# Kernel tuning notes

Measured on AMD Instinct MI355X. Metric: run time of the kernel, lower is better.

Reference implementation:

```python
import jax, jax.numpy as jnp
import numpy as np
import math

R = 3; NTOT = 100000; N0 = 80000; N1 = 20000; B = 4096
E1 = 300000; E2 = 65536
F_IN = 128; HID = 128; H1 = 2; OUT = 128
HC1 = H1 * HID   # 256
HC2 = OUT        # 128 (heads=1 in layer 2)


def setup_inputs() -> dict:
    key = jax.random.key(0)
    ks = jax.random.split(key, 40)
    w = lambda i, shape: (jax.random.normal(ks[i], shape, jnp.float32) * 0.05)
    inp = {}
    inp['features'] = jax.random.normal(ks[0], (NTOT, F_IN), jnp.float32)
    inp['n_ids'] = jax.random.randint(ks[1], (R, N0), 0, NTOT)
    src1 = jax.random.randint(ks[2], (R, 1, E1), 0, N0)
    dst1 = jax.random.randint(ks[3], (R, 1, E1), 0, N1)
    inp['ei1'] = jnp.concatenate([src1, dst1], axis=1)
    src2 = jax.random.randint(ks[4], (R, 1, E2), 0, N1)
    dst2 = jax.random.randint(ks[5], (R, 1, E2), 0, B)
    inp['ei2'] = jnp.concatenate([src2, dst2], axis=1)
    inp['wq1'] = w(6, (R, F_IN, HC1)); inp['bq1'] = w(7, (R, HC1))
    inp['wk1'] = w(8, (R, F_IN, HC1)); inp['bk1'] = w(9, (R, HC1))
    inp['wv1'] = w(10, (R, F_IN, HC1)); inp['bv1'] = w(11, (R, HC1))
    inp['ws1'] = w(12, (R, F_IN, HC1)); inp['bs1'] = w(13, (R, HC1))
    inp['wbeta1'] = w(14, (R, 3 * HC1, 1))
    # batchnorm (eval mode, running stats)
    inp['bn_g'] = jax.random.uniform(ks[15], (R, HC1), jnp.float32, 0.5, 1.5)
    inp['bn_b'] = w(16, (R, HC1))
    inp['bn_m'] = w(17, (R, HC1))
    inp['bn_v'] = jax.random.uniform(ks[18], (R, HC1), jnp.float32, 0.5, 1.5)
    inp['wq2'] = w(19, (R, HC1, HC2)); inp['bq2'] = w(20, (R, HC2))
    inp['wk2'] = w(21, (R, HC1, HC2)); inp['bk2'] = w(22, (R, HC2))
    inp['wv2'] = w(23, (R, HC1, HC2)); inp['bv2'] = w(24, (R, HC2))
    inp['ws2'] = w(25, (R, HC1, HC2)); inp['bs2'] = w(26, (R, HC2))
    inp['wbeta2'] = w(27, (R, 3 * HC2, 1))
    return inp


def transformer_conv(x_src, x_dst, src, dst, wq, bq, wk, bk, wv, bv, ws, bs, wbeta, H, C, Nt):
    """PyG TransformerConv, bipartite, concat=True, beta=True, eval (no dropout)."""
    q = (x_dst @ wq + bq).reshape(-1, H, C)   # [Nt, H, C]
    k = (x_src @ wk + bk).reshape(-1, H, C)   # [Ns, H, C]
    v = (x_src @ wv + bv).reshape(-1, H, C)
    # per-edge attention logits
    alpha = jnp.einsum('ehc,ehc->eh', q[dst], k[src]) / math.sqrt(C)  # [E, H]
    amax = jax.ops.segment_max(alpha, dst, num_segments=Nt)           # [Nt, H]
    amax = jnp.where(jnp.isfinite(amax), amax, 0.0)
    p = jnp.exp(alpha - amax[dst])
    denom = jax.ops.segment_sum(p, dst, num_segments=Nt)              # [Nt, H]
    p = p / denom[dst]
    out = jax.ops.segment_sum(p[:, :, None] * v[src], dst, num_segments=Nt)
    out = out.reshape(Nt, H * C)
    x_r = x_dst @ ws + bs                                             # skip connection
    beta = jax.nn.sigmoid(jnp.concatenate([out, x_r, out - x_r], -1) @ wbeta)  # [Nt,1]
    return beta * x_r + (1.0 - beta) * out


def reference(features, n_ids, ei1, ei2,
              wq1, bq1, wk1, bk1, wv1, bv1, ws1, bs1, wbeta1,
              bn_g, bn_b, bn_m, bn_v,
              wq2, bq2, wk2, bk2, wv2, bv2, ws2, bs2, wbeta2):
    outs = []
    for r in range(R):
        x = features[n_ids[r]]                 # [N0, 128]
        h = transformer_conv(x, x[:N1], ei1[r, 0], ei1[r, 1],
                             wq1[r], bq1[r], wk1[r], bk1[r], wv1[r], bv1[r],
                             ws1[r], bs1[r], wbeta1[r], H1, HID, N1)  # [N1, 256]
        h = (h - bn_m[r]) * jax.lax.rsqrt(bn_v[r] + 1e-5) * bn_g[r] + bn_b[r]
        h = jax.nn.elu(h)
        o = transformer_conv(h, h[:B], ei2[r, 0], ei2[r, 1],
                             wq2[r], bq2[r], wk2[r], bk2[r], wv2[r], bv2[r],
                             ws2[r], bs2[r], wbeta2[r], 1, OUT, B)    # [B, 128]
        outs.append(o)
    feats = jnp.stack(outs, 0)                 # [R, B, 128]
    return jnp.transpose(feats, (1, 0, 2)).reshape(B, R * OUT)
```

## Files before the change

kernel.cpp:

```cpp
#include <hip/hip_runtime.h>
#include <math.h>

#define RR 3
#define NTOT 100000
#define NN0 80000
#define NN1 20000
#define NB 4096
#define NE1 300000
#define NE2 65536
#define FIN 128
#define HC1 256
#define HC2 128

typedef __attribute__((ext_vector_type(8))) short bf16x8;
typedef __attribute__((ext_vector_type(4))) short s16x4;
typedef __attribute__((ext_vector_type(2))) short s16x2;
typedef __attribute__((ext_vector_type(4))) float f32x4;
typedef __attribute__((ext_vector_type(2))) float f32x2;

__device__ __forceinline__ float wave_red_sum(float v) {
    #pragma unroll
    for (int off = 32; off >= 1; off >>= 1) v += __shfl_xor(v, off, 64);
    return v;
}

__device__ __forceinline__ short f2bf(float x) {
    union { float f; unsigned u; } c; c.f = x;
    unsigned r = c.u + 0x7fffu + ((c.u >> 16) & 1u);
    return (short)(r >> 16);
}
__device__ __forceinline__ float bf2f(short s) {
    union { unsigned u; float f; } c; c.u = ((unsigned)(unsigned short)s) << 16;
    return c.f;
}

__device__ __forceinline__ float4 dec_fp8x4(unsigned w) {
    f32x2 lo = __builtin_amdgcn_cvt_pk_f32_fp8((int)w, false);
    f32x2 hi = __builtin_amdgcn_cvt_pk_f32_fp8((int)w, true);
    float4 r = { lo[0], lo[1], hi[0], hi[1] };
    return r;
}
__device__ __forceinline__ float2 dec_fp8x2(unsigned w) {
    f32x2 lo = __builtin_amdgcn_cvt_pk_f32_fp8((int)w, false);
    float2 r = { lo[0], lo[1] };
    return r;
}
__device__ __forceinline__ unsigned enc_fp8x4(float a, float b, float c, float d) {
    int w = __builtin_amdgcn_cvt_pk_fp8_f32(a, b, 0, false);
    w = __builtin_amdgcn_cvt_pk_fp8_f32(c, d, w, true);
    return (unsigned)w;
}

__device__ __forceinline__ float4 ld4(const float* p) { return *(const float4*)p; }
__device__ __forceinline__ float4 ld4(const short* p) {
    s16x4 v = *(const s16x4*)p;
    float4 r = { bf2f(v[0]), bf2f(v[1]), bf2f(v[2]), bf2f(v[3]) };
    return r;
}
__device__ __forceinline__ float2 ld2(const float* p) { return *(const float2*)p; }
__device__ __forceinline__ float2 ld2(const short* p) {
    s16x2 v = *(const s16x2*)p;
    float2 r = { bf2f(v[0]), bf2f(v[1]) };
    return r;
}

__global__ void __launch_bounds__(256)
fcvt_k(const float* __restrict__ f, short* __restrict__ o, int n4) {
    int i = blockIdx.x * 256 + threadIdx.x;
    if (i < n4) {
        float4 v = *(const float4*)(f + (size_t)i * 4);
        s16x4 s = { f2bf(v.x), f2bf(v.y), f2bf(v.z), f2bf(v.w) };
        *(s16x4*)(o + (size_t)i * 4) = s;
    }
}

template<int K, int N>
__global__ void __launch_bounds__(256)
wpack_k(const float* __restrict__ W0, const float* __restrict__ W1,
        const float* __restrict__ W2, const float* __restrict__ W3,
        short* __restrict__ P) {
    constexpr int KS = K / 32;
    const int m = blockIdx.y, r = blockIdx.z;
    const float* W = (m == 0 ? W0 : m == 1 ? W1 : m == 2 ? W2 : W3) + (size_t)r * K * N;
    short* o = P + ((size_t)(r * 4 + m)) * K * N;
    for (int i = blockIdx.x * 256 + threadIdx.x; i < K * N; i += gridDim.x * 256) {
        int j = i & 7, lane = (i >> 3) & 63, f = i >> 9;
        int ks = f % KS, nt = f / KS;
        int k = ks * 32 + (lane >> 4) * 8 + j;
        int n = nt * 16 + (lane & 15);
        o[i] = f2bf(W[(size_t)k * N + n]);
    }
}

template<int K, int N, typename OT0, typename OT1>
__global__ void __launch_bounds__(256)
gemm2l(const short* __restrict__ xbf, int ldx, const int* __restrict__ gidx,
       const short* __restrict__ P0, const float* __restrict__ b0, OT0* __restrict__ out0,
       const short* __restrict__ P1, const float* __restrict__ b1, OT1* __restrict__ out1)
{
    constexpr int NT = N / 16;
    constexpr int NW = NT / 4;
    constexpr int KS = K / 32;
    constexpr int MT = 2;
    const int lane = threadIdx.x & 63;
    const int wid  = threadIdx.x >> 6;
    const int rowbase = blockIdx.x * (MT * 16);

    const short* ap[MT];
    #pragma unroll
    for (int mt = 0; mt < MT; ++mt) {
        int arow = rowbase + mt * 16 + (lane & 15);
        int srow = gidx ? gidx[arow] : arow;
        ap[mt] = xbf + (size_t)srow * ldx + ((lane >> 4) * 8);
    }
    const int fb = lane * 8;

    f32x4 acc[MT][NW][2];
    #pragma unroll
    for (int mt = 0; mt < MT; ++mt)
        #pragma unroll
        for (int j = 0; j < NW; ++j) { acc[mt][j][0] = (f32x4)(0.0f); acc[mt][j][1] = (f32x4)(0.0f); }

    for (int ks = 0; ks < KS; ++ks) {
        bf16x8 a[MT];
        #pragma unroll
        for (int mt = 0; mt < MT; ++mt) a[mt] = *(const bf16x8*)(ap[mt] + ks * 32);
        #pragma unroll
        for (int j = 0; j < NW; ++j) {
            const int nt = wid * NW + j;
            const int off = ((nt * KS + ks) << 9) + fb;
            bf16x8 bv0 = *(const bf16x8*)(P0 + off);
            bf16x8 bv1 = *(const bf16x8*)(P1 + off);
            #pragma unroll
            for (int mt = 0; mt < MT; ++mt) {
                acc[mt][j][0] = __builtin_amdgcn_mfma_f32_16x16x32_bf16(a[mt], bv0, acc[mt][j][0], 0, 0, 0);
                acc[mt][j][1] = __builtin_amdgcn_mfma_f32_16x16x32_bf16(a[mt], bv1, acc[mt][j][1], 0, 0, 0);
            }
        }
    }

    __shared__ float ls[MT * 16][N + 4];
    constexpr int CPT = (MT * 16) * N / 8 / 256;
    const int tid = threadIdx.x;

    #pragma unroll
    for (int mat = 0; mat < 2; ++mat) {
        if (mat) __syncthreads();
        const float* bias = mat ? b1 : b0;
        #pragma unroll
        for (int j = 0; j < NW; ++j) {
            const int nt = wid * NW + j;
            const float bb = bias[nt * 16 + (lane & 15)];
            #pragma unroll
            for (int mt = 0; mt < MT; ++mt)
                #pragma unroll
                for (int rg = 0; rg < 4; ++rg)
                    ls[mt * 16 + (lane >> 4) * 4 + rg][nt * 16 + (lane & 15)] =
                        acc[mt][j][mat][rg] + bb;
        }
        __syncthreads();
        #pragma unroll
        for (int c2 = 0; c2 < CPT; ++c2) {
            const int chunk = c2 * 256 + tid;
            const int row = chunk / (N / 8);
            const int colb = (chunk % (N / 8)) * 8;
            float v[8];
            #pragma unroll
            for (int i = 0; i < 8; ++i) v[i] = ls[row][colb + i];
            const size_t gbase = (size_t)(rowbase + row) * N + colb;
            if (mat == 0) {
                if constexpr (sizeof(OT0) == 1) {
                    uint2 u = { enc_fp8x4(v[0],v[1],v[2],v[3]), enc_fp8x4(v[4],v[5],v[6],v[7]) };
                    *(uint2*)((unsigned char*)out0 + gbase) = u;
                } else if constexpr (sizeof(OT0) == 2) {
                    bf16x8 s;
                    #pragma unroll
                    for (int i = 0; i < 8; ++i) s[i] = f2bf(v[i]);
                    *(bf16x8*)(out0 + gbase) = s;
                } else {
                    float4 lo = { v[0], v[1], v[2], v[3] }, hi = { v[4], v[5], v[6], v[7] };
                    *(float4*)(out0 + gbase) = lo;
                    *(float4*)(out0 + gbase + 4) = hi;
                }
            } else {
                if constexpr (sizeof(OT1) == 1) {
                    uint2 u = { enc_fp8x4(v[0],v[1],v[2],v[3]), enc_fp8x4(v[4],v[5],v[6],v[7]) };
                    *(uint2*)((unsigned char*)out1 + gbase) = u;
                } else if constexpr (sizeof(OT1) == 2) {
                    bf16x8 s;
                    #pragma unroll
                    for (int i = 0; i < 8; ++i) s[i] = f2bf(v[i]);
                    *(bf16x8*)(out1 + gbase) = s;
                } else {
                    float4 lo = { v[0], v[1], v[2], v[3] }, hi = { v[4], v[5], v[6], v[7] };
                    *(float4*)(out1 + gbase) = lo;
                    *(float4*)(out1 + gbase + 4) = hi;
                }
            }
        }
    }
}

template<int TS>
__global__ void __launch_bounds__(256)
csr_a1(const int* __restrict__ ei, int E, int R, int T, int* __restrict__ cnt_tr) {
    const int r = blockIdx.y, tile = blockIdx.x;
    const int* dst = ei + (size_t)r * 2 * E + E;
    __shared__ int h[64];
    for (int i = threadIdx.x; i < R; i += 256) h[i] = 0;
    __syncthreads();
    const int e0 = tile * TS, e1 = min(e0 + TS, E);
    for (int e = e0 + threadIdx.x; e < e1; e += 256) atomicAdd(&h[dst[e] >> 9], 1);
    __syncthreads();
    for (int i = threadIdx.x; i < R; i += 256)
        cnt_tr[((size_t)r * R + i) * T + tile] = h[i];
}
__global__ void __launch_bounds__(64)
csr_b(const int* __restrict__ cnt_tr, int R, int T, int E, int nbins,
      int* __restrict__ base_tr, int* __restrict__ rbase, int* __restrict__ offsg) {
    const int r = blockIdx.x;
    __shared__ int tot[64];
    const int t = threadIdx.x;
    if (t < R) {
        const int* c = cnt_tr + ((size_t)r * R + t) * T;
        int s = 0;
        for (int i = 0; i < T; ++i) s += c[i];
        tot[t] = s;
    }
    __syncthreads();
    if (t == 0) { int run = 0; for (int i = 0; i < R; ++i) { int c = tot[i]; tot[i] = run; run += c; } }
    __syncthreads();
    if (t < R) {
        const int* c = cnt_tr + ((size_t)r * R + t) * T;
        int* b = base_tr + ((size_t)r * R + t) * T;
        int run = tot[t];
        for (int i = 0; i < T; ++i) { b[i] = run; run += c[i]; }
        rbase[(size_t)r * (R + 1) + t] = tot[t];
    }
    if (t == 0) {
        rbase[(size_t)r * (R + 1) + R] = E;
        offsg[(size_t)r * (nbins + 1) + nbins] = E;
    }
}
template<int TS>
__global__ void __launch_bounds__(256)
csr_a2(const int* __restrict__ ei, int E, int R, int T,
       const int* __restrict__ base_tr, unsigned long long* __restrict__ scratch) {
    const int r = blockIdx.y, tile = blockIdx.x;
    const int* src = ei + (size_t)r * 2 * E;
    const int* dst = src + E;
    __shared__ int cur[64];
    for (int i = threadIdx.x; i < R; i += 256)
        cur[i] = base_tr[((size_t)r * R + i) * T + tile];
    __syncthreads();
    unsigned long long* sc = scratch + (size_t)r * E;
    const int e0 = tile * TS, e1 = min(e0 + TS, E);
    for (int e = e0 + threadIdx.x; e < e1; e += 256) {
        int d = dst[e];
        int pos = atomicAdd(&cur[d >> 9], 1);
        sc[pos] = ((unsigned long long)(unsigned)d << 32) | (unsigned)src[e];
    }
}
__global__ void __launch_bounds__(256)
csr_c(const unsigned long long* __restrict__ scratch, const int* __restrict__ rbase,
      int E, int R, int nbins, int* __restrict__ offsg, int* __restrict__ slistg) {
    const int r = blockIdx.y, range = blockIdx.x;
    const unsigned long long* sc = scratch + (size_t)r * E;
    const int* rb = rbase + (size_t)r * (R + 1);
    int* offs = offsg + (size_t)r * (nbins + 1);
    int* slist = slistg + (size_t)r * E;
    const int s0 = rb[range], s1 = rb[range + 1];
    const int lo = range << 9;
    const int nb = min(512, nbins - lo);
    __shared__ int h0[512];
    __shared__ int cur[512];
    __shared__ int ps[256];
    const int tid = threadIdx.x;
    h0[2*tid] = 0; h0[2*tid+1] = 0;
    __syncthreads();
    for (int i = s0 + tid; i < s1; i += 256)
        atomicAdd(&h0[(int)(sc[i] >> 32) - lo], 1);
    __syncthreads();
    const int a_ = h0[2*tid], b_ = h0[2*tid+1];
    ps[tid] = a_ + b_;
    __syncthreads();
    for (int off = 1; off < 256; off <<= 1) {
        int v = (tid >= off) ? ps[tid - off] : 0;
        __syncthreads();
        ps[tid] += v;
        __syncthreads();
    }
    const int base = (tid ? ps[tid - 1] : 0) + s0;
    const int o0 = base, o1 = base + a_;
    if (2*tid     < nb) offs[lo + 2*tid]     = o0;
    if (2*tid + 1 < nb) offs[lo + 2*tid + 1] = o1;
    cur[2*tid] = o0; cur[2*tid+1] = o1;
    __syncthreads();
    for (int i = s0 + tid; i < s1; i += 256) {
        unsigned long long v = sc[i];
        int d = (int)(v >> 32) - lo;
        int pos = atomicAdd(&cur[d], 1);
        slist[pos] = (int)(v & 0xffffffffu);
    }
}

__global__ void __launch_bounds__(64)
attn1_k(const int* __restrict__ offs, const int* __restrict__ slist,
        const short* __restrict__ qb, const unsigned char* __restrict__ kb,
        const short* __restrict__ vb,
        const short* __restrict__ xr, const float* __restrict__ wb,
        const float* __restrict__ g, const float* __restrict__ bbn,
        const float* __restrict__ mean, const float* __restrict__ var,
        short* __restrict__ hb)
{
    const int n = blockIdx.x;
    const int lane = threadIdx.x;
    const int c0 = lane * 4;
    const int lo = offs[n], hi = offs[n+1];
    const float4 q = ld4(qb + (size_t)n * HC1 + c0);
    const float scale = 0.088388347648318447f;

    float m = -INFINITY, s = 0.f;
    float a0 = 0.f, a1 = 0.f, a2 = 0.f, a3 = 0.f;
    unsigned kw0 = 0, kw1 = 0;
    float4 v0 = {0,0,0,0}, v1 = {0,0,0,0};
    if (lo < hi) {
        int sr = slist[lo];
        kw0 = *(const unsigned*)(kb + (size_t)sr * HC1 + c0);
        v0 = ld4(vb + (size_t)sr * HC1 + c0);
    }
    if (lo + 1 < hi) {
        int sr = slist[lo + 1];
        kw1 = *(const unsigned*)(kb + (size_t)sr * HC1 + c0);
        v1 = ld4(vb + (size_t)sr * HC1 + c0);
    }
    for (int i = lo; i < hi; i += 2) {
        unsigned kwn0 = 0, kwn1 = 0;
        float4 vn0 = {0,0,0,0}, vn1 = {0,0,0,0};
        if (i + 2 < hi) {
            int sr = slist[i + 2];
            kwn0 = *(const unsigned*)(kb + (size_t)sr * HC1 + c0);
            vn0 = ld4(vb + (size_t)sr * HC1 + c0);
        }
        if (i + 3 < hi) {
            int sr = slist[i + 3];
            kwn1 = *(const unsigned*)(kb + (size_t)sr * HC1 + c0);
            vn1 = ld4(vb + (size_t)sr * HC1 + c0);
        }
        const float4 k0 = dec_fp8x4(kw0);
        const float4 k1 = dec_fp8x4(kw1);
        float p0 = q.x*k0.x + q.y*k0.y + q.z*k0.z + q.w*k0.w;
        float p1 = q.x*k1.x + q.y*k1.y + q.z*k1.z + q.w*k1.w;
        #pragma unroll
        for (int off = 16; off >= 1; off >>= 1) {
            p0 += __shfl_xor(p0, off, 64);
            p1 += __shfl_xor(p1, off, 64);
        }
        const float alpha0 = p0 * scale;
        const float alpha1 = (i + 1 < hi) ? p1 * scale : -INFINITY;
        float mn = fmaxf(m, alpha0);
        float rs = __expf(m - mn);
        float pp = __expf(alpha0 - mn);
        s  = s*rs + pp;
        a0 = a0*rs + pp*v0.x; a1 = a1*rs + pp*v0.y;
        a2 = a2*rs + pp*v0.z; a3 = a3*rs + pp*v0.w;
        m = mn;
        mn = fmaxf(m, alpha1);
        rs = __expf(m - mn);
        pp = __expf(alpha1 - mn);
        s  = s*rs + pp;
        a0 = a0*rs + pp*v1.x; a1 = a1*rs + pp*v1.y;
        a2 = a2*rs + pp*v1.z; a3 = a3*rs + pp*v1.w;
        m = mn;
        kw0 = kwn0; v0 = vn0; kw1 = kwn1; v1 = vn1;
    }
    const float inv = (s > 0.f) ? 1.f/s : 0.f;
    const float att[4] = { a0*inv, a1*inv, a2*inv, a3*inv };

    const float4 x4 = ld4(xr + (size_t)n * HC1 + c0);
    const float xx[4] = { x4.x, x4.y, x4.z, x4.w };
    float d = 0.f;
    #pragma unroll
    for (int j = 0; j < 4; ++j) {
        int c = c0 + j;
        d += att[j]*wb[c] + xx[j]*wb[HC1 + c] + (att[j]-xx[j])*wb[2*HC1 + c];
    }
    d = wave_red_sum(d);
    const float beta = 1.f / (1.f + __expf(-d));
    s16x4 hv4;
    #pragma unroll
    for (int j = 0; j < 4; ++j) {
        int c = c0 + j;
        float hv = beta*xx[j] + (1.f-beta)*att[j];
        hv = (hv - mean[c]) * rsqrtf(var[c] + 1e-5f) * g[c] + bbn[c];
        hv = hv > 0.f ? hv : expm1f(hv);
        hv4[j] = f2bf(hv);
    }
    *(s16x4*)(hb + (size_t)n * HC1 + c0) = hv4;
}

__global__ void __launch_bounds__(64)
attn2_k(const int* __restrict__ offs, const int* __restrict__ slist,
        const short* __restrict__ qb, const unsigned char* __restrict__ kb,
        const short* __restrict__ vb,
        const short* __restrict__ xr, const float* __restrict__ wb,
        float* __restrict__ outp, int colofs)
{
    const int n = blockIdx.x;
    const int lane = threadIdx.x;
    const int c0 = lane * 2;
    const int lo = offs[n], hi = offs[n+1];
    const float2 q = ld2(qb + (size_t)n * HC2 + c0);
    const float scale = 0.088388347648318447f;

    float m = -INFINITY, s = 0.f;
    float a0 = 0.f, a1 = 0.f;
    unsigned kw0 = 0, kw1 = 0;
    float2 v0 = {0,0}, v1 = {0,0};
    if (lo < hi) {
        int sr = slist[lo];
        kw0 = *(const unsigned short*)(kb + (size_t)sr * HC2 + c0);
        v0 = ld2(vb + (size_t)sr * HC2 + c0);
    }
    if (lo + 1 < hi) {
        int sr = slist[lo + 1];
        kw1 = *(const unsigned short*)(kb + (size_t)sr * HC2 + c0);
        v1 = ld2(vb + (size_t)sr * HC2 + c0);
    }
    for (int i = lo; i < hi; i += 2) {
        unsigned kwn0 = 0, kwn1 = 0;
        float2 vn0 = {0,0}, vn1 = {0,0};
        if (i + 2 < hi) {
            int sr = slist[i + 2];
            kwn0 = *(const unsigned short*)(kb + (size_t)sr * HC2 + c0);
            vn0 = ld2(vb + (size_t)sr * HC2 + c0);
        }
        if (i + 3 < hi) {
            int sr = slist[i + 3];
            kwn1 = *(const unsigned short*)(kb + (size_t)sr * HC2 + c0);
            vn1 = ld2(vb + (size_t)sr * HC2 + c0);
        }
        const float2 k0 = dec_fp8x2(kw0);
        const float2 k1 = dec_fp8x2(kw1);
        float p0 = q.x*k0.x + q.y*k0.y;
        float p1 = q.x*k1.x + q.y*k1.y;
        #pragma unroll
        for (int off = 32; off >= 1; off >>= 1) {
            p0 += __shfl_xor(p0, off, 64);
            p1 += __shfl_xor(p1, off, 64);
        }
        const float alpha0 = p0 * scale;
        const float alpha1 = (i + 1 < hi) ? p1 * scale : -INFINITY;
        float mn = fmaxf(m, alpha0);
        float rs = __expf(m - mn);
        float pp = __expf(alpha0 - mn);
        s  = s*rs + pp;
        a0 = a0*rs + pp*v0.x; a1 = a1*rs + pp*v0.y;
        m = mn;
        mn = fmaxf(m, alpha1);
        rs = __expf(m - mn);
        pp = __expf(alpha1 - mn);
        s  = s*rs + pp;
        a0 = a0*rs + pp*v1.x; a1 = a1*rs + pp*v1.y;
        m = mn;
        kw0 = kwn0; v0 = vn0; kw1 = kwn1; v1 = vn1;
    }
    const float inv = (s > 0.f) ? 1.f/s : 0.f;
    const float att0 = a0*inv, att1 = a1*inv;

    const float2 x2 = ld2(xr + (size_t)n * HC2 + c0);
    float d = att0*wb[c0] + att1*wb[c0+1]
            + x2.x*wb[HC2+c0] + x2.y*wb[HC2+c0+1]
            + (att0-x2.x)*wb[2*HC2+c0] + (att1-x2.y)*wb[2*HC2+c0+1];
    d = wave_red_sum(d);
    const float beta = 1.f/(1.f+__expf(-d));
    outp[(size_t)n*(RR*HC2) + colofs + c0]     = beta*x2.x + (1.f-beta)*att0;
    outp[(size_t)n*(RR*HC2) + colofs + c0 + 1] = beta*x2.y + (1.f-beta)*att1;
}

extern "C" void kernel_launch(void* const* d_in, const int* in_sizes, int n_in,
                              void* d_out, int out_size, void* d_ws, size_t ws_size,
                              hipStream_t stream)
{
    const float* features = (const float*)d_in[0];
    const int*   n_ids    = (const int*)d_in[1];
    const int*   ei1      = (const int*)d_in[2];
    const int*   ei2      = (const int*)d_in[3];
    const float* wq1 = (const float*)d_in[4];  const float* bq1 = (const float*)d_in[5];
    const float* wk1 = (const float*)d_in[6];  const float* bk1 = (const float*)d_in[7];
    const float* wv1 = (const float*)d_in[8];  const float* bv1 = (const float*)d_in[9];
    const float* ws1 = (const float*)d_in[10]; const float* bs1 = (const float*)d_in[11];
    const float* wbeta1 = (const float*)d_in[12];
    const float* bn_g = (const float*)d_in[13]; const float* bn_b = (const float*)d_in[14];
    const float* bn_m = (const float*)d_in[15]; const float* bn_v = (const float*)d_in[16];
    const float* wq2 = (const float*)d_in[17]; const float* bq2 = (const float*)d_in[18];
    const float* wk2 = (const float*)d_in[19]; const float* bk2 = (const float*)d_in[20];
    const float* wv2 = (const float*)d_in[21]; const float* bv2 = (const float*)d_in[22];
    const float* ws2 = (const float*)d_in[23]; const float* bs2 = (const float*)d_in[24];
    const float* wbeta2 = (const float*)d_in[25];
    float* outp = (float*)d_out;

    constexpr int TS = 8192;
    constexpr int T1 = (NE1 + TS - 1) / TS;
    constexpr int T2 = (NE2 + TS - 1) / TS;
    constexpr int R1 = (NN1 + 511) >> 9;
    constexpr int R2 = (NB  + 511) >> 9;

    char* p = (char*)d_ws;
    auto alloc = [&](size_t bytes) { char* q = p; p += (bytes + 255) & ~(size_t)255; return q; };
    unsigned char* k1b = (unsigned char*)alloc((size_t)NN0*HC1);
    short* v1b  = (short*)alloc(sizeof(short)*(size_t)NN0*HC1);
    short* q1b  = (short*)alloc(sizeof(short)*(size_t)NN1*HC1);
    short* xr1  = (short*)alloc(sizeof(short)*(size_t)NN1*HC1);
    short* hbf  = (short*)alloc(sizeof(short)*(size_t)NN1*HC1);
    short* xbf  = (short*)alloc(sizeof(short)*(size_t)NTOT*FIN);
    short* wt1  = (short*)alloc(sizeof(short)*(size_t)RR*4*FIN*HC1);
    short* wt2  = (short*)alloc(sizeof(short)*(size_t)RR*4*HC1*HC2);
    unsigned char* k2b = (unsigned char*)alloc((size_t)NN1*HC2);
    short* v2b  = (short*)alloc(sizeof(short)*(size_t)NN1*HC2);
    short* q2b  = (short*)alloc(sizeof(short)*(size_t)NB*HC2);
    short* xr2  = (short*)alloc(sizeof(short)*(size_t)NB*HC2);
    int* offs1  = (int*)alloc(sizeof(int)*(size_t)RR*(NN1+1));
    int* slist1 = (int*)alloc(sizeof(int)*(size_t)RR*NE1);
    int* offs2  = (int*)alloc(sizeof(int)*(size_t)RR*(NB+1));
    int* slist2 = (int*)alloc(sizeof(int)*(size_t)RR*NE2);
    unsigned long long* scr1 = (unsigned long long*)alloc(sizeof(unsigned long long)*(size_t)RR*NE1);
    unsigned long long* scr2 = (unsigned long long*)alloc(sizeof(unsigned long long)*(size_t)RR*NE2);
    int* cnt_tr1  = (int*)alloc(sizeof(int)*(size_t)RR*R1*T1);
    int* base_tr1 = (int*)alloc(sizeof(int)*(size_t)RR*R1*T1);
    int* rbase1   = (int*)alloc(sizeof(int)*(size_t)RR*(R1+1));
    int* cnt_tr2  = (int*)alloc(sizeof(int)*(size_t)RR*R2*T2);
    int* base_tr2 = (int*)alloc(sizeof(int)*(size_t)RR*R2*T2);
    int* rbase2   = (int*)alloc(sizeof(int)*(size_t)RR*(R2+1));
    (void)ws_size; (void)in_sizes; (void)n_in; (void)out_size;

    fcvt_k<<<(NTOT*FIN/4 + 255)/256, 256, 0, stream>>>(features, xbf, NTOT*FIN/4);
    {
        dim3 g1(128, 4, RR);
        wpack_k<FIN, HC1><<<g1, 256, 0, stream>>>(wq1, wk1, wv1, ws1, wt1);
        dim3 g2(128, 4, RR);
        wpack_k<HC1, HC2><<<g2, 256, 0, stream>>>(wq2, wk2, wv2, ws2, wt2);
    }

    {
        dim3 ga1(T1, RR), ga2(T2, RR);
        csr_a1<TS><<<ga1, 256, 0, stream>>>(ei1, NE1, R1, T1, cnt_tr1);
        csr_a1<TS><<<ga2, 256, 0, stream>>>(ei2, NE2, R2, T2, cnt_tr2);
        csr_b<<<RR, 64, 0, stream>>>(cnt_tr1, R1, T1, NE1, NN1, base_tr1, rbase1, offs1);
        csr_b<<<RR, 64, 0, stream>>>(cnt_tr2, R2, T2, NE2, NB,  base_tr2, rbase2, offs2);
        csr_a2<TS><<<ga1, 256, 0, stream>>>(ei1, NE1, R1, T1, base_tr1, scr1);
        csr_a2<TS><<<ga2, 256, 0, stream>>>(ei2, NE2, R2, T2, base_tr2, scr2);
        dim3 gc1(R1, RR), gc2(R2, RR);
        csr_c<<<gc1, 256, 0, stream>>>(scr1, rbase1, NE1, R1, NN1, offs1, slist1);
        csr_c<<<gc2, 256, 0, stream>>>(scr2, rbase2, NE2, R2, NB,  offs2, slist2);
    }

    const size_t WSZ = (size_t)FIN*HC1;

    for (int r = 0; r < RR; ++r) {
        const int* nid  = n_ids + (size_t)r*NN0;
        const short* ptq1 = wt1 + ((size_t)r*4 + 0)*WSZ;
        const short* ptk1 = wt1 + ((size_t)r*4 + 1)*WSZ;
        const short* ptv1 = wt1 + ((size_t)r*4 + 2)*WSZ;
        const short* pts1 = wt1 + ((size_t)r*4 + 3)*WSZ;
        const short* ptq2 = wt2 + ((size_t)r*4 + 0)*WSZ;
        const short* ptk2 = wt2 + ((size_t)r*4 + 1)*WSZ;
        const short* ptv2 = wt2 + ((size_t)r*4 + 2)*WSZ;
        const short* pts2 = wt2 + ((size_t)r*4 + 3)*WSZ;

        gemm2l<FIN, HC1, unsigned char, short><<<NN0/32, 256, 0, stream>>>(
            xbf, FIN, nid, ptk1, bk1 + r*HC1, k1b, ptv1, bv1 + r*HC1, v1b);
        gemm2l<FIN, HC1, short, short><<<NN1/32, 256, 0, stream>>>(
            xbf, FIN, nid, ptq1, bq1 + r*HC1, q1b, pts1, bs1 + r*HC1, xr1);

        attn1_k<<<NN1, 64, 0, stream>>>(offs1 + (size_t)r*(NN1+1), slist1 + (size_t)r*NE1,
            q1b, k1b, v1b, xr1,
            wbeta1 + (size_t)r*3*HC1,
            bn_g + (size_t)r*HC1, bn_b + (size_t)r*HC1,
            bn_m + (size_t)r*HC1, bn_v + (size_t)r*HC1, hbf);

        gemm2l<HC1, HC2, unsigned char, short><<<NN1/32, 256, 0, stream>>>(
            hbf, HC1, nullptr, ptk2, bk2 + r*HC2, k2b, ptv2, bv2 + r*HC2, v2b);
        gemm2l<HC1, HC2, short, short><<<NB/32, 256, 0, stream>>>(
            hbf, HC1, nullptr, ptq2, bq2 + r*HC2, q2b, pts2, bs2 + r*HC2, xr2);

        attn2_k<<<NB, 64, 0, stream>>>(offs2 + (size_t)r*(NB+1), slist2 + (size_t)r*NE2,
            q2b, k2b, v2b, xr2,
            wbeta2 + (size_t)r*3*HC2, outp, r*HC2);
    }
}
```

Baseline: 516.8 us.

## Pre-partition layer-1 edges by source bucket before the destination CSR sort

Adds a first counting-sort pass that groups layer-1 edges into source-index buckets (2048-node ranges), then runs the existing destination-bucket partition on that pre-grouped stream. Each destination segment then holds edges roughly ordered by source, so the later gathers of K and V rows during attention should hit cache better. In exchange it adds three kernel launches, an extra scratch buffer, and another full read and write of the edge list.

```diff
diff --git a/kernel.cpp b/kernel.cpp
--- a/kernel.cpp
+++ b/kernel.cpp
@@ -201,6 +201,7 @@
     }
 }
 
+
 template<int TS>
 __global__ void __launch_bounds__(256)
 csr_a1(const int* __restrict__ ei, int E, int R, int T, int* __restrict__ cnt_tr) {
@@ -211,6 +212,34 @@
     __syncthreads();
     const int e0 = tile * TS, e1 = min(e0 + TS, E);
     for (int e = e0 + threadIdx.x; e < e1; e += 256) atomicAdd(&h[dst[e] >> 9], 1);
+    __syncthreads();
+    for (int i = threadIdx.x; i < R; i += 256)
+        cnt_tr[((size_t)r * R + i) * T + tile] = h[i];
+}
+template<int TS, int SSH>
+__global__ void __launch_bounds__(256)
+seg_a1(const int* __restrict__ ei, int E, int R, int T, int* __restrict__ cnt_tr) {
+    const int r = blockIdx.y, tile = blockIdx.x;
+    const int* src = ei + (size_t)r * 2 * E;
+    __shared__ int h[64];
+    for (int i = threadIdx.x; i < R; i += 256) h[i] = 0;
+    __syncthreads();
+    const int e0 = tile * TS, e1 = min(e0 + TS, E);
+    for (int e = e0 + threadIdx.x; e < e1; e += 256) atomicAdd(&h[src[e] >> SSH], 1);
+    __syncthreads();
+    for (int i = threadIdx.x; i < R; i += 256)
+        cnt_tr[((size_t)r * R + i) * T + tile] = h[i];
+}
+template<int TS>
+__global__ void __launch_bounds__(256)
+csr_a1p(const unsigned long long* __restrict__ scr_s, int E, int R, int T, int* __restrict__ cnt_tr) {
+    const int r = blockIdx.y, tile = blockIdx.x;
+    const unsigned long long* sc = scr_s + (size_t)r * E;
+    __shared__ int h[64];
+    for (int i = threadIdx.x; i < R; i += 256) h[i] = 0;
+    __syncthreads();
+    const int e0 = tile * TS, e1 = min(e0 + TS, E);
+    for (int e = e0 + threadIdx.x; e < e1; e += 256) atomicAdd(&h[(int)(sc[e] >> 32) >> 9], 1);
     __syncthreads();
     for (int i = threadIdx.x; i < R; i += 256)
         cnt_tr[((size_t)r * R + i) * T + tile] = h[i];
@@ -240,6 +269,43 @@
     if (t == 0) {
         rbase[(size_t)r * (R + 1) + R] = E;
         offsg[(size_t)r * (nbins + 1) + nbins] = E;
+    }
+}
+template<int TS, int SSH>
+__global__ void __launch_bounds__(256)
+seg_a2(const int* __restrict__ ei, int E, int R, int T,
+       const int* __restrict__ base_tr, unsigned long long* __restrict__ scr_s) {
+    const int r = blockIdx.y, tile = blockIdx.x;
+    const int* src = ei + (size_t)r * 2 * E;
+    const int* dst = src + E;
+    __shared__ int cur[64];
+    for (int i = threadIdx.x; i < R; i += 256)
+        cur[i] = base_tr[((size_t)r * R + i) * T + tile];
+    __syncthreads();
+    unsigned long long* sc = scr_s + (size_t)r * E;
+    const int e0 = tile * TS, e1 = min(e0 + TS, E);
+    for (int e = e0 + threadIdx.x; e < e1; e += 256) {
+        int s = src[e];
+        int pos = atomicAdd(&cur[s >> SSH], 1);
+        sc[pos] = ((unsigned long long)(unsigned)dst[e] << 32) | (unsigned)s;
+    }
+}
+template<int TS>
+__global__ void __launch_bounds__(256)
+csr_a2p(const unsigned long long* __restrict__ scr_s, int E, int R, int T,
+        const int* __restrict__ base_tr, unsigned long long* __restrict__ scratch) {
+    const int r = blockIdx.y, tile = blockIdx.x;
+    const unsigned long long* in = scr_s + (size_t)r * E;
+    __shared__ int cur[64];
+    for (int i = threadIdx.x; i < R; i += 256)
+        cur[i] = base_tr[((size_t)r * R + i) * T + tile];
+    __syncthreads();
+    unsigned long long* sc = scratch + (size_t)r * E;
+    const int e0 = tile * TS, e1 = min(e0 + TS, E);
+    for (int e = e0 + threadIdx.x; e < e1; e += 256) {
+        unsigned long long v = in[e];
+        int pos = atomicAdd(&cur[(int)(v >> 32) >> 9], 1);
+        sc[pos] = v;
     }
 }
 template<int TS>
@@ -505,6 +571,8 @@
     constexpr int T2 = (NE2 + TS - 1) / TS;
     constexpr int R1 = (NN1 + 511) >> 9;
     constexpr int R2 = (NB  + 511) >> 9;
+    constexpr int SSH = 11;
+    constexpr int RS1 = (NN0 + (1 << SSH) - 1) >> SSH;
 
     char* p = (char*)d_ws;
     auto alloc = [&](size_t bytes) { char* q = p; p += (bytes + 255) & ~(size_t)255; return q; };
@@ -524,14 +592,19 @@
     int* slist1 = (int*)alloc(sizeof(int)*(size_t)RR*NE1);
     int* offs2  = (int*)alloc(sizeof(int)*(size_t)RR*(NB+1));
     int* slist2 = (int*)alloc(sizeof(int)*(size_t)RR*NE2);
-    unsigned long long* scr1 = (unsigned long long*)alloc(sizeof(unsigned long long)*(size_t)RR*NE1);
-    unsigned long long* scr2 = (unsigned long long*)alloc(sizeof(unsigned long long)*(size_t)RR*NE2);
+    unsigned long long* scr1  = (unsigned long long*)alloc(sizeof(unsigned long long)*(size_t)RR*NE1);
+    unsigned long long* scrs1 = (unsigned long long*)alloc(sizeof(unsigned long long)*(size_t)RR*NE1);
+    unsigned long long* scr2  = (unsigned long long*)alloc(sizeof(unsigned long long)*(size_t)RR*NE2);
     int* cnt_tr1  = (int*)alloc(sizeof(int)*(size_t)RR*R1*T1);
     int* base_tr1 = (int*)alloc(sizeof(int)*(size_t)RR*R1*T1);
     int* rbase1   = (int*)alloc(sizeof(int)*(size_t)RR*(R1+1));
     int* cnt_tr2  = (int*)alloc(sizeof(int)*(size_t)RR*R2*T2);
     int* base_tr2 = (int*)alloc(sizeof(int)*(size_t)RR*R2*T2);
     int* rbase2   = (int*)alloc(sizeof(int)*(size_t)RR*(R2+1));
+    int* cnt_sr1  = (int*)alloc(sizeof(int)*(size_t)RR*RS1*T1);
+    int* base_sr1 = (int*)alloc(sizeof(int)*(size_t)RR*RS1*T1);
+    int* rbase_s1 = (int*)alloc(sizeof(int)*(size_t)RR*(RS1+1));
+    int* dummy1   = (int*)alloc(sizeof(int)*(size_t)RR*(RS1+1));
     (void)ws_size; (void)in_sizes; (void)n_in; (void)out_size;
 
     fcvt_k<<<(NTOT*FIN/4 + 255)/256, 256, 0, stream>>>(features, xbf, NTOT*FIN/4);
@@ -544,11 +617,14 @@
 
     {
         dim3 ga1(T1, RR), ga2(T2, RR);
-        csr_a1<TS><<<ga1, 256, 0, stream>>>(ei1, NE1, R1, T1, cnt_tr1);
+        seg_a1<TS, SSH><<<ga1, 256, 0, stream>>>(ei1, NE1, RS1, T1, cnt_sr1);
+        csr_b<<<RR, 64, 0, stream>>>(cnt_sr1, RS1, T1, NE1, RS1, base_sr1, rbase_s1, dummy1);
+        seg_a2<TS, SSH><<<ga1, 256, 0, stream>>>(ei1, NE1, RS1, T1, base_sr1, scrs1);
+        csr_a1p<TS><<<ga1, 256, 0, stream>>>(scrs1, NE1, R1, T1, cnt_tr1);
+        csr_b<<<RR, 64, 0, stream>>>(cnt_tr1, R1, T1, NE1, NN1, base_tr1, rbase1, offs1);
+        csr_a2p<TS><<<ga1, 256, 0, stream>>>(scrs1, NE1, R1, T1, base_tr1, scr1);
         csr_a1<TS><<<ga2, 256, 0, stream>>>(ei2, NE2, R2, T2, cnt_tr2);
-        csr_b<<<RR, 64, 0, stream>>>(cnt_tr1, R1, T1, NE1, NN1, base_tr1, rbase1, offs1);
         csr_b<<<RR, 64, 0, stream>>>(cnt_tr2, R2, T2, NE2, NB,  base_tr2, rbase2, offs2);
-        csr_a2<TS><<<ga1, 256, 0, stream>>>(ei1, NE1, R1, T1, base_tr1, scr1);
         csr_a2<TS><<<ga2, 256, 0, stream>>>(ei2, NE2, R2, T2, base_tr2, scr2);
         dim3 gc1(R1, RR), gc2(R2, RR);
         csr_c<<<gc1, 256, 0, stream>>>(scr1, rbase1, NE1, R1, NN1, offs1, slist1);
```

Measured after the change: 544.5 us. 5.4% more time.
